# Kernel optimization log

Hardware: AMD Instinct MI355X
Metric: run time of the kernel (lower is better)

## Reference

```python
import jax, jax.numpy as jnp
import numpy as np

D_MODEL = 1024
NUM_HEADS = 16
HEAD_DIM = D_MODEL // NUM_HEADS
THETA = 10000.0
B, S = 4, 2048


def _rope(x, pos):
    # x: [B, H, S, d], pos: [B, S] int
    half = HEAD_DIM // 2
    inv_freq = THETA ** (-(jnp.arange(half, dtype=jnp.float32) * 2.0) / HEAD_DIM)  # [half]
    ang = pos.astype(jnp.float32)[:, None, :, None] * inv_freq  # [B, 1, S, half]
    cos, sin = jnp.cos(ang), jnp.sin(ang)
    x1, x2 = x[..., 0::2], x[..., 1::2]  # interleaved pairs
    r1 = x1 * cos - x2 * sin
    r2 = x1 * sin + x2 * cos
    return jnp.stack([r1, r2], axis=-1).reshape(x.shape)


def setup_inputs() -> dict:
    key = jax.random.key(0)
    ks = jax.random.split(key, 12)
    scale = 1.0 / np.sqrt(D_MODEL)
    inp = {
        "query": jax.random.normal(ks[0], (B, S, D_MODEL), dtype=jnp.float32),
        "key": jax.random.normal(ks[1], (B, S, D_MODEL), dtype=jnp.float32),
        "value": jax.random.normal(ks[2], (B, S, D_MODEL), dtype=jnp.float32),
        "token_positions": jnp.broadcast_to(jnp.arange(S, dtype=jnp.int32), (B, S)),
        "w_q": jax.random.normal(ks[3], (D_MODEL, D_MODEL), dtype=jnp.float32) * scale,
        "b_q": jnp.zeros((D_MODEL,), dtype=jnp.float32),
        "w_k": jax.random.normal(ks[4], (D_MODEL, D_MODEL), dtype=jnp.float32) * scale,
        "b_k": jnp.zeros((D_MODEL,), dtype=jnp.float32),
        "w_v": jax.random.normal(ks[5], (D_MODEL, D_MODEL), dtype=jnp.float32) * scale,
        "b_v": jnp.zeros((D_MODEL,), dtype=jnp.float32),
        "w_o": jax.random.normal(ks[6], (D_MODEL, D_MODEL), dtype=jnp.float32) * scale,
        "b_o": jnp.zeros((D_MODEL,), dtype=jnp.float32),
    }
    return inp


def reference(query, key, value, token_positions, w_q, b_q, w_k, b_k, w_v, b_v, w_o, b_o):
    b, s, _ = query.shape
    Q = query @ w_q + b_q
    K = key @ w_k + b_k
    V = value @ w_v + b_v
    # [B, S, H, d] -> [B, H, S, d]
    Q = Q.reshape(b, s, NUM_HEADS, HEAD_DIM).transpose(0, 2, 1, 3)
    K = K.reshape(b, s, NUM_HEADS, HEAD_DIM).transpose(0, 2, 1, 3)
    V = V.reshape(b, s, NUM_HEADS, HEAD_DIM).transpose(0, 2, 1, 3)
    Q = _rope(Q, token_positions)
    K = _rope(K, token_positions)
    scores = jnp.einsum("bhqd,bhkd->bhqk", Q, K) / jnp.sqrt(jnp.float32(HEAD_DIM))
    causal = jnp.tril(jnp.ones((s, s), dtype=bool))
    scores = jnp.where(causal, scores, -jnp.inf)
    attn = jax.nn.softmax(scores, axis=-1)
    out = jnp.einsum("bhqk,bhkd->bhqd", attn, V)
    out = out.transpose(0, 2, 1, 3).reshape(b, s, D_MODEL)
    return out @ w_o + b_o
```

## Files before the change

kernel.cpp:

```cpp
#include <hip/hip_runtime.h>

typedef __bf16 bf16;
typedef __attribute__((ext_vector_type(8))) __bf16 bf16x8;
typedef __attribute__((ext_vector_type(4))) __bf16 bf16x4;
typedef __attribute__((ext_vector_type(4))) float floatx4;

#define MFMA16(a, b, c) __builtin_amdgcn_mfma_f32_16x16x32_bf16((a), (b), (c), 0, 0, 0)

#define GLL(g, l)                                                   \
  __builtin_amdgcn_global_load_lds(                                 \
      (const __attribute__((address_space(1))) void*)(g),           \
      (__attribute__((address_space(3))) void*)(l), 16, 0, 0)

static constexpr int DM = 1024;
static constexpr int SEQ = 2048;
static constexpr int BATCH = 4;
static constexpr int NH = 16;
static constexpr int HD = 64;
static constexpr float LOG2E = 1.4426950408889634f;
static constexpr float LOG2_THETA = 13.287712379549449f;
static constexpr float QSC = 0.125f * LOG2E;

__global__ __launch_bounds__(256) void convert_x(
    const float* __restrict__ q, const float* __restrict__ k,
    const float* __restrict__ v, bf16* __restrict__ qo,
    bf16* __restrict__ ko, bf16* __restrict__ vo) {
  int z = blockIdx.z;
  const float* src = (z == 0) ? q : (z == 1) ? k : v;
  bf16* dst = (z == 0) ? qo : (z == 1) ? ko : vo;
  size_t i = ((size_t)blockIdx.x * blockDim.x + threadIdx.x) * 8;
  float4 a = *(const float4*)(src + i);
  float4 b = *(const float4*)(src + i + 4);
  bf16x8 o;
  o[0] = (bf16)a.x; o[1] = (bf16)a.y; o[2] = (bf16)a.z; o[3] = (bf16)a.w;
  o[4] = (bf16)b.x; o[5] = (bf16)b.y; o[6] = (bf16)b.z; o[7] = (bf16)b.w;
  *(bf16x8*)(dst + i) = o;
}

__global__ __launch_bounds__(256) void convert_w(
    const float* __restrict__ wq, const float* __restrict__ wk,
    const float* __restrict__ wv, const float* __restrict__ wo,
    bf16* __restrict__ oq, bf16* __restrict__ ok, bf16* __restrict__ ov,
    bf16* __restrict__ oo) {
  int z = blockIdx.z;
  const float* src = (z == 0) ? wq : (z == 1) ? wk : (z == 2) ? wv : wo;
  bf16* dst = (z == 0) ? oq : (z == 1) ? ok : (z == 2) ? ov : oo;
  __shared__ __align__(16) bf16 T[64][72];
  int k0 = blockIdx.y * 64, n0 = blockIdx.x * 64;
  int tid = threadIdx.x;
  int r = tid >> 4, c4 = (tid & 15) * 4;
#pragma unroll
  for (int i = 0; i < 4; i++) {
    int kk = r + i * 16;
    float4 v = *(const float4*)(src + (size_t)(k0 + kk) * DM + n0 + c4);
    T[c4 + 0][kk] = (bf16)v.x;
    T[c4 + 1][kk] = (bf16)v.y;
    T[c4 + 2][kk] = (bf16)v.z;
    T[c4 + 3][kk] = (bf16)v.w;
  }
  __syncthreads();
#pragma unroll
  for (int i = 0; i < 4; i++) {
    int nn = r + i * 16;
    bf16x4 o = *(const bf16x4*)&T[nn][c4];
    *(bf16x4*)(dst + (size_t)(n0 + nn) * DM + k0 + c4) = o;
  }
}

__global__ __launch_bounds__(256) void rope_table(const int* __restrict__ tp,
                                                  float* __restrict__ tab) {
  int idx = blockIdx.x * 256 + threadIdx.x;
  int m = idx >> 5, i = idx & 31;
  float pos = (float)tp[m];
  float invf = exp2f(-(float)(2 * i) * (LOG2_THETA / 64.0f));
  float s, c;
  sincosf(pos * invf, &s, &c);
  tab[(size_t)idx * 2] = c;
  tab[(size_t)idx * 2 + 1] = s;
}

__global__ __launch_bounds__(256) void gemm_qkv(
    const bf16* __restrict__ qb, const bf16* __restrict__ kb,
    const bf16* __restrict__ vb, const bf16* __restrict__ wqt,
    const bf16* __restrict__ wkt, const bf16* __restrict__ wvt,
    const float* __restrict__ biq, const float* __restrict__ bik,
    const float* __restrict__ biv, const float* __restrict__ tab,
    bf16* __restrict__ Qr, bf16* __restrict__ Kr, bf16* __restrict__ Vr) {
  int z = blockIdx.z;
  const bf16* X = (z == 0) ? qb : (z == 1) ? kb : vb;
  const bf16* Wt = (z == 0) ? wqt : (z == 1) ? wkt : wvt;
  const float* bias = (z == 0) ? biq : (z == 1) ? bik : biv;

  __shared__ __align__(16) bf16 As[128 * 64];
  __shared__ __align__(16) bf16 Bs[128 * 64];
  int lin = blockIdx.x;
  int m0 = (lin & 63) * 128, n0 = (lin >> 6) * 128;
  int tid = threadIdx.x;
  int lane = tid & 63, wv = tid >> 6;
  int quad = lane >> 4, low = lane & 15;
  int wm = (wv >> 1) * 64, wn = (wv & 1) * 64;
  int lr8 = lane >> 3;
  int swcol = ((lane & 7) ^ lr8) * 8;
  const bf16* AgL = X + (size_t)(m0 + wv * 8 + lr8) * DM + swcol;
  const bf16* BgL = Wt + (size_t)(n0 + wv * 8 + lr8) * DM + swcol;
  bf16* AsL = As + wv * 8 * 64;
  bf16* BsL = Bs + wv * 8 * 64;
  int r3 = low & 7;

  floatx4 acc[4][4];
#pragma unroll
  for (int i = 0; i < 4; i++)
#pragma unroll
    for (int j = 0; j < 4; j++) acc[i][j] = (floatx4)0.0f;

  for (int kt = 0; kt < DM; kt += 64) {
#pragma unroll
    for (int c = 0; c < 4; c++) {
      GLL(AgL + kt + (size_t)(c * 32) * DM, AsL + c * 2048);
      GLL(BgL + kt + (size_t)(c * 32) * DM, BsL + c * 2048);
    }
    __syncthreads();
#pragma unroll
    for (int kc = 0; kc < 2; kc++) {
      bf16x8 xf[4], wf[4];
#pragma unroll
      for (int t = 0; t < 4; t++)
        xf[t] = *(const bf16x8*)&As[(wm + t * 16 + low) * 64 +
                                    (((kc << 2) | quad) ^ r3) * 8];
#pragma unroll
      for (int t = 0; t < 4; t++)
        wf[t] = *(const bf16x8*)&Bs[(wn + t * 16 + low) * 64 +
                                    (((kc << 2) | quad) ^ r3) * 8];
#pragma unroll
      for (int i = 0; i < 4; i++)
#pragma unroll
        for (int j = 0; j < 4; j++)
          acc[i][j] = MFMA16(wf[i], xf[j], acc[i][j]);
    }
    __syncthreads();
  }

#pragma unroll
  for (int i = 0; i < 4; i++) {
    int nb = n0 + wn + i * 16 + quad * 4;
    float4 bv = *(const float4*)(bias + nb);
    int h = nb >> 6, dbase = nb & 63;
#pragma unroll
    for (int j = 0; j < 4; j++) {
      int m = m0 + wm + j * 16 + low;
      int bb = m >> 11, ss = m & 2047;
      float v0 = acc[i][j][0] + bv.x;
      float v1 = acc[i][j][1] + bv.y;
      float v2 = acc[i][j][2] + bv.z;
      float v3 = acc[i][j][3] + bv.w;
      size_t off = ((size_t)(bb * NH + h) * SEQ + ss) * HD + dbase;
      bf16x4 pk;
      if (z < 2) {
        float4 cs = *(const float4*)(tab + (size_t)m * 64 + dbase);
        float o0 = v0 * cs.x - v1 * cs.y;
        float o1 = v0 * cs.y + v1 * cs.x;
        float o2 = v2 * cs.z - v3 * cs.w;
        float o3 = v2 * cs.w + v3 * cs.z;
        if (z == 0) { o0 *= QSC; o1 *= QSC; o2 *= QSC; o3 *= QSC; }
        pk[0] = (bf16)o0; pk[1] = (bf16)o1;
        pk[2] = (bf16)o2; pk[3] = (bf16)o3;
        bf16* dst = (z == 0) ? Qr : Kr;
        *(bf16x4*)(dst + off) = pk;
      } else {
        pk[0] = (bf16)v0; pk[1] = (bf16)v1;
        pk[2] = (bf16)v2; pk[3] = (bf16)v3;
        *(bf16x4*)(Vr + off) = pk;
      }
    }
  }
}

__global__ __launch_bounds__(256) void transpose_v(const bf16* __restrict__ Vr,
                                                   bf16* __restrict__ Vt) {
  int bh = blockIdx.y;
  int s0 = blockIdx.x * 64;
  __shared__ __align__(16) bf16 T[64][72];
  int t = threadIdx.x;
  int r = t >> 2, c = (t & 3) * 16;
  const bf16* src = Vr + ((size_t)bh * SEQ + s0 + r) * HD + c;
  bf16x8 a = *(const bf16x8*)src;
  bf16x8 b = *(const bf16x8*)(src + 8);
  *(bf16x8*)&T[r][c] = a;
  *(bf16x8*)&T[r][c + 8] = b;
  __syncthreads();
  bf16* dst = Vt + ((size_t)bh * HD + r) * SEQ + s0 + c;
  bf16x8 o0, o1;
#pragma unroll
  for (int j = 0; j < 8; j++) {
    o0[j] = T[c + j][r];
    o1[j] = T[c + 8 + j][r];
  }
  *(bf16x8*)dst = o0;
  *(bf16x8*)(dst + 8) = o1;
}

__global__ __launch_bounds__(256, 3) void attn_fa(const bf16* __restrict__ Qr,
                                                  const bf16* __restrict__ Kr,
                                                  const bf16* __restrict__ Vt,
                                                  bf16* __restrict__ attn) {
  int lin = blockIdx.x;
  int bh = lin & 63, qi = 15 - (lin >> 6);
  int ntiles = 2 * qi + 2;
  int tid = threadIdx.x, lane = tid & 63, w = tid >> 6;
  int quad = lane >> 4, low = lane & 15;
  __shared__ __align__(16) bf16 Ks[2][64 * 72];
  __shared__ __align__(16) bf16 Vs[2][64 * 72];
  __shared__ __align__(16) bf16 Pl[4][16 * 72];
  const bf16* Qh = Qr + (size_t)bh * SEQ * HD;
  const bf16* Kh = Kr + (size_t)bh * SEQ * HD;
  const bf16* Vh = Vt + (size_t)bh * HD * SEQ;
  int bb = bh >> 4, h = bh & 15;
  int qrow0 = qi * 128 + w * 32;

  int sr = tid >> 2, scol = (tid & 3) * 16;
  const bf16* Kg = Kh + (size_t)sr * HD + scol;
  const bf16* Vg = Vh + (size_t)sr * SEQ + scol;
  int sl = sr * 72 + scol;

  bf16x8 ones;
#pragma unroll
  for (int j = 0; j < 8; j++) ones[j] = (bf16)1.0f;

  bf16x8 aq[2][2];
#pragma unroll
  for (int rt = 0; rt < 2; rt++)
#pragma unroll
    for (int kc = 0; kc < 2; kc++)
      aq[rt][kc] = *(const bf16x8*)(Qh + (size_t)(qrow0 + rt * 16 + low) * HD +
                                    kc * 32 + quad * 8);

  floatx4 accO[2][4];
  floatx4 lacc[2];
#pragma unroll
  for (int rt = 0; rt < 2; rt++) {
    lacc[rt] = (floatx4)0.0f;
#pragma unroll
    for (int nt = 0; nt < 4; nt++) accO[rt][nt] = (floatx4)0.0f;
  }

  {
    bf16x8 k0 = *(const bf16x8*)(Kg);
    bf16x8 k1 = *(const bf16x8*)(Kg + 8);
    bf16x8 v0 = *(const bf16x8*)(Vg);
    bf16x8 v1 = *(const bf16x8*)(Vg + 8);
    *(bf16x8*)&Ks[0][sl] = k0;
    *(bf16x8*)&Ks[0][sl + 8] = k1;
    *(bf16x8*)&Vs[0][sl] = v0;
    *(bf16x8*)&Vs[0][sl + 8] = v1;
  }
  __syncthreads();

  for (int kt = 0; kt < ntiles; kt++) {
    int cur = kt & 1;
    bf16x8 nk0, nk1, nv0, nv1;
    bool pre = (kt + 1 < ntiles);
    if (pre) {
      const bf16* kg = Kg + (size_t)(kt + 1) * (64 * HD);
      const bf16* vg = Vg + (size_t)(kt + 1) * 64;
      nk0 = *(const bf16x8*)(kg);
      nk1 = *(const bf16x8*)(kg + 8);
      nv0 = *(const bf16x8*)(vg);
      nv1 = *(const bf16x8*)(vg + 8);
    }

    floatx4 s2[2][4];
#pragma unroll
    for (int rt = 0; rt < 2; rt++)
#pragma unroll
      for (int nt = 0; nt < 4; nt++) s2[rt][nt] = (floatx4)0.0f;
#pragma unroll
    for (int nt = 0; nt < 4; nt++) {
      bf16x8 kb0 = *(const bf16x8*)&Ks[cur][(nt * 16 + low) * 72 + quad * 8];
      bf16x8 kb1 =
          *(const bf16x8*)&Ks[cur][(nt * 16 + low) * 72 + 32 + quad * 8];
#pragma unroll
      for (int rt = 0; rt < 2; rt++) {
        s2[rt][nt] = MFMA16(kb0, aq[rt][0], s2[rt][nt]);
        s2[rt][nt] = MFMA16(kb1, aq[rt][1], s2[rt][nt]);
      }
    }
    if (kt >= ntiles - 2) {
#pragma unroll
      for (int nt = 0; nt < 4; nt++)
#pragma unroll
        for (int r = 0; r < 4; r++) {
          int kg_ = kt * 64 + nt * 16 + quad * 4 + r;
#pragma unroll
          for (int rt = 0; rt < 2; rt++) {
            int qg = qrow0 + rt * 16 + low;
            if (kg_ > qg) s2[rt][nt][r] = -INFINITY;
          }
        }
    }
    bf16x4 pk[2][4];
#pragma unroll
    for (int rt = 0; rt < 2; rt++)
#pragma unroll
      for (int nt = 0; nt < 4; nt++)
#pragma unroll
        for (int r = 0; r < 4; r++)
          pk[rt][nt][r] = (bf16)exp2f(s2[rt][nt][r]);
    bf16x8 vb0[4], vb1[4];
#pragma unroll
    for (int nt = 0; nt < 4; nt++) {
      vb0[nt] = *(const bf16x8*)&Vs[cur][(nt * 16 + low) * 72 + quad * 8];
      vb1[nt] = *(const bf16x8*)&Vs[cur][(nt * 16 + low) * 72 + 32 + quad * 8];
    }
#pragma unroll
    for (int rt = 0; rt < 2; rt++) {
#pragma unroll
      for (int nt = 0; nt < 4; nt++)
        *(bf16x4*)&Pl[w][low * 72 + nt * 16 + quad * 4] = pk[rt][nt];
      asm volatile("s_waitcnt lgkmcnt(0)" ::: "memory");
      bf16x8 ap0 = *(const bf16x8*)&Pl[w][low * 72 + quad * 8];
      bf16x8 ap1 = *(const bf16x8*)&Pl[w][low * 72 + 32 + quad * 8];
#pragma unroll
      for (int nt = 0; nt < 4; nt++) {
        accO[rt][nt] = MFMA16(ap0, vb0[nt], accO[rt][nt]);
        accO[rt][nt] = MFMA16(ap1, vb1[nt], accO[rt][nt]);
      }
      lacc[rt] = MFMA16(ap0, ones, lacc[rt]);
      lacc[rt] = MFMA16(ap1, ones, lacc[rt]);
    }
    if (pre) {
      int nb = cur ^ 1;
      *(bf16x8*)&Ks[nb][sl] = nk0;
      *(bf16x8*)&Ks[nb][sl + 8] = nk1;
      *(bf16x8*)&Vs[nb][sl] = nv0;
      *(bf16x8*)&Vs[nb][sl + 8] = nv1;
    }
    __syncthreads();
  }

#pragma unroll
  for (int rt = 0; rt < 2; rt++)
#pragma unroll
    for (int r = 0; r < 4; r++) {
      float inv = 1.0f / lacc[rt][r];
      int q = qrow0 + rt * 16 + quad * 4 + r;
#pragma unroll
      for (int nt = 0; nt < 4; nt++) {
        float o = accO[rt][nt][r] * inv;
        attn[((size_t)(bb * SEQ + q)) * DM + h * HD + nt * 16 + low] = (bf16)o;
      }
    }
}

__global__ __launch_bounds__(256) void gemm_out(const bf16* __restrict__ X,
                                                const bf16* __restrict__ Wt,
                                                const float* __restrict__ bias,
                                                float* __restrict__ out) {
  __shared__ __align__(16) bf16 As[128 * 64];
  __shared__ __align__(16) bf16 Bs[128 * 64];
  int lin = blockIdx.x;
  int m0 = (lin & 63) * 128, n0 = (lin >> 6) * 128;
  int tid = threadIdx.x;
  int lane = tid & 63, wv = tid >> 6;
  int quad = lane >> 4, low = lane & 15;
  int wm = (wv >> 1) * 64, wn = (wv & 1) * 64;
  int lr8 = lane >> 3;
  int swcol = ((lane & 7) ^ lr8) * 8;
  const bf16* AgL = X + (size_t)(m0 + wv * 8 + lr8) * DM + swcol;
  const bf16* BgL = Wt + (size_t)(n0 + wv * 8 + lr8) * DM + swcol;
  bf16* AsL = As + wv * 8 * 64;
  bf16* BsL = Bs + wv * 8 * 64;
  int r3 = low & 7;

  floatx4 acc[4][4];
#pragma unroll
  for (int i = 0; i < 4; i++)
#pragma unroll
    for (int j = 0; j < 4; j++) acc[i][j] = (floatx4)0.0f;

  for (int kt = 0; kt < DM; kt += 64) {
#pragma unroll
    for (int c = 0; c < 4; c++) {
      GLL(AgL + kt + (size_t)(c * 32) * DM, AsL + c * 2048);
      GLL(BgL + kt + (size_t)(c * 32) * DM, BsL + c * 2048);
    }
    __syncthreads();
#pragma unroll
    for (int kc = 0; kc < 2; kc++) {
      bf16x8 xf[4], wf[4];
#pragma unroll
      for (int t = 0; t < 4; t++)
        xf[t] = *(const bf16x8*)&As[(wm + t * 16 + low) * 64 +
                                    (((kc << 2) | quad) ^ r3) * 8];
#pragma unroll
      for (int t = 0; t < 4; t++)
        wf[t] = *(const bf16x8*)&Bs[(wn + t * 16 + low) * 64 +
                                    (((kc << 2) | quad) ^ r3) * 8];
#pragma unroll
      for (int i = 0; i < 4; i++)
#pragma unroll
        for (int j = 0; j < 4; j++)
          acc[i][j] = MFMA16(wf[i], xf[j], acc[i][j]);
    }
    __syncthreads();
  }

#pragma unroll
  for (int i = 0; i < 4; i++) {
    int nb = n0 + wn + i * 16 + quad * 4;
    float4 bv = *(const float4*)(bias + nb);
#pragma unroll
    for (int j = 0; j < 4; j++) {
      int m = m0 + wm + j * 16 + low;
      float4 o;
      o.x = acc[i][j][0] + bv.x;
      o.y = acc[i][j][1] + bv.y;
      o.z = acc[i][j][2] + bv.z;
      o.w = acc[i][j][3] + bv.w;
      *(float4*)(out + (size_t)m * DM + nb) = o;
    }
  }
}

extern "C" void kernel_launch(void* const* d_in, const int* in_sizes, int n_in,
                              void* d_out, int out_size, void* d_ws,
                              size_t ws_size, hipStream_t stream) {
  const float* query = (const float*)d_in[0];
  const float* key_ = (const float*)d_in[1];
  const float* value = (const float*)d_in[2];
  const int* tp = (const int*)d_in[3];
  const float* w_q = (const float*)d_in[4];
  const float* b_q = (const float*)d_in[5];
  const float* w_k = (const float*)d_in[6];
  const float* b_k = (const float*)d_in[7];
  const float* w_v = (const float*)d_in[8];
  const float* b_v = (const float*)d_in[9];
  const float* w_o = (const float*)d_in[10];
  const float* b_o = (const float*)d_in[11];

  char* w = (char*)d_ws;
  const size_t MB = 1u << 20;
  bf16* qb = (bf16*)(w + 0);
  bf16* kb = (bf16*)(w + 16 * MB);
  bf16* vb = (bf16*)(w + 32 * MB);
  bf16* wqt = (bf16*)(w + 48 * MB);
  bf16* wkt = (bf16*)(w + 50 * MB);
  bf16* wvt = (bf16*)(w + 52 * MB);
  bf16* wot = (bf16*)(w + 54 * MB);
  bf16* Qr = (bf16*)(w + 56 * MB);
  bf16* Kr = (bf16*)(w + 72 * MB);
  bf16* Vr = (bf16*)(w + 88 * MB);
  float* tab = (float*)(w + 104 * MB);
  bf16* Vt = (bf16*)(w + 32 * MB);
  bf16* attnb = (bf16*)(w + 0);

  convert_x<<<dim3(4096, 1, 3), 256, 0, stream>>>(query, key_, value, qb, kb,
                                                  vb);
  convert_w<<<dim3(16, 16, 4), 256, 0, stream>>>(w_q, w_k, w_v, w_o, wqt, wkt,
                                                 wvt, wot);
  rope_table<<<1024, 256, 0, stream>>>(tp, tab);
  gemm_qkv<<<dim3(512, 1, 3), 256, 0, stream>>>(qb, kb, vb, wqt, wkt, wvt,
                                                b_q, b_k, b_v, tab, Qr, Kr,
                                                Vr);
  transpose_v<<<dim3(32, 64), 256, 0, stream>>>(Vr, Vt);
  attn_fa<<<dim3(1024), 256, 0, stream>>>(Qr, Kr, Vt, attnb);
  gemm_out<<<dim3(512), 256, 0, stream>>>(attnb, wot, b_o, (float*)d_out);
}
```

Baseline: 330.8 us.

## Triple-buffer GEMM tiles with async LDS prefetch and larger 256x128 blocks

Replaces the single-buffered GEMM loop in the QKV and output projections with a shared gemm_core. It keeps three LDS stages and issues global_load_lds prefetches two k-tiles ahead, split across the two half-k steps. Explicit vmcnt/lgkmcnt waits, s_barrier and setprio bracket the MFMA blocks so that loads overlap compute. Block size grows to 512 threads with a 256x128 tile, which halves the grid and increases reuse of the weight tile. The cost is about 144KB of LDS per block, so only one block fits per CU, and the tile count now roughly matches the CU count, which risks load imbalance and low occupancy.

```diff
diff --git a/kernel.cpp b/kernel.cpp
--- a/kernel.cpp
+++ b/kernel.cpp
@@ -17,6 +17,7 @@
 static constexpr int BATCH = 4;
 static constexpr int NH = 16;
 static constexpr int HD = 64;
+static constexpr int NT = DM / 64;
 static constexpr float LOG2E = 1.4426950408889634f;
 static constexpr float LOG2_THETA = 13.287712379549449f;
 static constexpr float QSC = 0.125f * LOG2E;
@@ -79,7 +80,114 @@
   tab[(size_t)idx * 2 + 1] = s;
 }
 
-__global__ __launch_bounds__(256) void gemm_qkv(
+__device__ __forceinline__ void gemm_core(const bf16* __restrict__ X,
+                                          const bf16* __restrict__ Wt,
+                                          bf16* As, bf16* Bs, int m0, int n0,
+                                          int tid, floatx4 acc[4][4]) {
+  int lane = tid & 63, wvq = tid >> 6;
+  int quad = lane >> 4, low = lane & 15;
+  int wm = (wvq >> 1) * 64, wn = (wvq & 1) * 64;
+  int lr8 = lane >> 3;
+  int swcol = ((lane & 7) ^ lr8) * 8;
+  const bf16* AgL = X + (size_t)(m0 + wvq * 8 + lr8) * DM + swcol;
+  const bf16* BgL = Wt + (size_t)(n0 + wvq * 8 + lr8) * DM + swcol;
+  bf16* AsW = As + wvq * 512;
+  bf16* BsW = Bs + wvq * 512;
+  int r3 = low & 7;
+
+#define GQ_A(kt2, b, r)                                            \
+  GLL(AgL + (size_t)(kt2) * 64 + (size_t)(r) * 64 * DM,            \
+      AsW + (b) * 16384 + (r) * 4096)
+#define GQ_B(kt2, b, r)                                            \
+  GLL(BgL + (size_t)(kt2) * 64 + (size_t)(r) * 64 * DM,            \
+      BsW + (b) * 8192 + (r) * 4096)
+
+#pragma unroll
+  for (int i = 0; i < 4; i++)
+#pragma unroll
+    for (int j = 0; j < 4; j++) acc[i][j] = (floatx4)0.0f;
+
+#pragma unroll
+  for (int r = 0; r < 4; r++) GQ_A(0, 0, r);
+#pragma unroll
+  for (int r = 0; r < 2; r++) GQ_B(0, 0, r);
+#pragma unroll
+  for (int r = 0; r < 4; r++) GQ_A(1, 1, r);
+#pragma unroll
+  for (int r = 0; r < 2; r++) GQ_B(1, 1, r);
+  asm volatile("s_waitcnt vmcnt(6)" ::: "memory");
+  __builtin_amdgcn_s_barrier();
+
+  int rb = 0;
+  for (int t = 0; t < NT; ++t) {
+    int sb = rb + 2;
+    if (sb > 2) sb -= 3;
+    const bf16* Ab = As + rb * 16384;
+    const bf16* Bb = Bs + rb * 8192;
+    bool st = (t < NT - 2);
+    bf16x8 wf[4], xf[4];
+#pragma unroll
+    for (int i = 0; i < 4; i++)
+      wf[i] = *(const bf16x8*)&Bb[(wn + i * 16 + low) * 64 + (quad ^ r3) * 8];
+#pragma unroll
+    for (int j = 0; j < 4; j++)
+      xf[j] = *(const bf16x8*)&Ab[(wm + j * 16 + low) * 64 + (quad ^ r3) * 8];
+    if (st) {
+      GQ_A(t + 2, sb, 0);
+      GQ_A(t + 2, sb, 1);
+      GQ_B(t + 2, sb, 0);
+    }
+    __builtin_amdgcn_sched_barrier(0);
+    __builtin_amdgcn_s_barrier();
+    asm volatile("s_waitcnt lgkmcnt(0)" ::: "memory");
+    __builtin_amdgcn_sched_barrier(0);
+    __builtin_amdgcn_s_setprio(1);
+#pragma unroll
+    for (int i = 0; i < 4; i++)
+#pragma unroll
+      for (int j = 0; j < 4; j++)
+        acc[i][j] = MFMA16(wf[i], xf[j], acc[i][j]);
+    __builtin_amdgcn_s_setprio(0);
+    __builtin_amdgcn_sched_barrier(0);
+    __builtin_amdgcn_s_barrier();
+#pragma unroll
+    for (int i = 0; i < 4; i++)
+      wf[i] =
+          *(const bf16x8*)&Bb[(wn + i * 16 + low) * 64 + ((4 | quad) ^ r3) * 8];
+#pragma unroll
+    for (int j = 0; j < 4; j++)
+      xf[j] =
+          *(const bf16x8*)&Ab[(wm + j * 16 + low) * 64 + ((4 | quad) ^ r3) * 8];
+    if (st) {
+      GQ_A(t + 2, sb, 2);
+      GQ_A(t + 2, sb, 3);
+      GQ_B(t + 2, sb, 1);
+    }
+    __builtin_amdgcn_sched_barrier(0);
+    __builtin_amdgcn_s_barrier();
+    asm volatile("s_waitcnt lgkmcnt(0)" ::: "memory");
+    __builtin_amdgcn_sched_barrier(0);
+    __builtin_amdgcn_s_setprio(1);
+#pragma unroll
+    for (int i = 0; i < 4; i++)
+#pragma unroll
+      for (int j = 0; j < 4; j++)
+        acc[i][j] = MFMA16(wf[i], xf[j], acc[i][j]);
+    __builtin_amdgcn_s_setprio(0);
+    if (st)
+      asm volatile("s_waitcnt vmcnt(6)" ::: "memory");
+    else
+      asm volatile("s_waitcnt vmcnt(0)" ::: "memory");
+    __builtin_amdgcn_sched_barrier(0);
+    __builtin_amdgcn_s_barrier();
+    rb = rb + 1;
+    if (rb > 2) rb -= 3;
+  }
+#undef GQ_A
+#undef GQ_B
+}
+
+__global__ __launch_bounds__(512) void gemm_qkv(
     const bf16* __restrict__ qb, const bf16* __restrict__ kb,
     const bf16* __restrict__ vb, const bf16* __restrict__ wqt,
     const bf16* __restrict__ wkt, const bf16* __restrict__ wvt,
@@ -91,54 +199,18 @@
   const bf16* Wt = (z == 0) ? wqt : (z == 1) ? wkt : wvt;
   const float* bias = (z == 0) ? biq : (z == 1) ? bik : biv;
 
-  __shared__ __align__(16) bf16 As[128 * 64];
-  __shared__ __align__(16) bf16 Bs[128 * 64];
+  __shared__ __align__(16) bf16 As[3 * 256 * 64];
+  __shared__ __align__(16) bf16 Bs[3 * 128 * 64];
   int lin = blockIdx.x;
-  int m0 = (lin & 63) * 128, n0 = (lin >> 6) * 128;
+  int m0 = (lin & 31) * 256, n0 = (lin >> 5) * 128;
   int tid = threadIdx.x;
-  int lane = tid & 63, wv = tid >> 6;
+
+  floatx4 acc[4][4];
+  gemm_core(X, Wt, As, Bs, m0, n0, tid, acc);
+
+  int lane = tid & 63, wvq = tid >> 6;
   int quad = lane >> 4, low = lane & 15;
-  int wm = (wv >> 1) * 64, wn = (wv & 1) * 64;
-  int lr8 = lane >> 3;
-  int swcol = ((lane & 7) ^ lr8) * 8;
-  const bf16* AgL = X + (size_t)(m0 + wv * 8 + lr8) * DM + swcol;
-  const bf16* BgL = Wt + (size_t)(n0 + wv * 8 + lr8) * DM + swcol;
-  bf16* AsL = As + wv * 8 * 64;
-  bf16* BsL = Bs + wv * 8 * 64;
-  int r3 = low & 7;
-
-  floatx4 acc[4][4];
-#pragma unroll
-  for (int i = 0; i < 4; i++)
-#pragma unroll
-    for (int j = 0; j < 4; j++) acc[i][j] = (floatx4)0.0f;
-
-  for (int kt = 0; kt < DM; kt += 64) {
-#pragma unroll
-    for (int c = 0; c < 4; c++) {
-      GLL(AgL + kt + (size_t)(c * 32) * DM, AsL + c * 2048);
-      GLL(BgL + kt + (size_t)(c * 32) * DM, BsL + c * 2048);
-    }
-    __syncthreads();
-#pragma unroll
-    for (int kc = 0; kc < 2; kc++) {
-      bf16x8 xf[4], wf[4];
-#pragma unroll
-      for (int t = 0; t < 4; t++)
-        xf[t] = *(const bf16x8*)&As[(wm + t * 16 + low) * 64 +
-                                    (((kc << 2) | quad) ^ r3) * 8];
-#pragma unroll
-      for (int t = 0; t < 4; t++)
-        wf[t] = *(const bf16x8*)&Bs[(wn + t * 16 + low) * 64 +
-                                    (((kc << 2) | quad) ^ r3) * 8];
-#pragma unroll
-      for (int i = 0; i < 4; i++)
-#pragma unroll
-        for (int j = 0; j < 4; j++)
-          acc[i][j] = MFMA16(wf[i], xf[j], acc[i][j]);
-    }
-    __syncthreads();
-  }
+  int wm = (wvq >> 1) * 64, wn = (wvq & 1) * 64;
 
 #pragma unroll
   for (int i = 0; i < 4; i++) {
@@ -351,58 +423,22 @@
     }
 }
 
-__global__ __launch_bounds__(256) void gemm_out(const bf16* __restrict__ X,
+__global__ __launch_bounds__(512) void gemm_out(const bf16* __restrict__ X,
                                                 const bf16* __restrict__ Wt,
                                                 const float* __restrict__ bias,
                                                 float* __restrict__ out) {
-  __shared__ __align__(16) bf16 As[128 * 64];
-  __shared__ __align__(16) bf16 Bs[128 * 64];
+  __shared__ __align__(16) bf16 As[3 * 256 * 64];
+  __shared__ __align__(16) bf16 Bs[3 * 128 * 64];
   int lin = blockIdx.x;
-  int m0 = (lin & 63) * 128, n0 = (lin >> 6) * 128;
+  int m0 = (lin & 31) * 256, n0 = (lin >> 5) * 128;
   int tid = threadIdx.x;
-  int lane = tid & 63, wv = tid >> 6;
+
+  floatx4 acc[4][4];
+  gemm_core(X, Wt, As, Bs, m0, n0, tid, acc);
+
+  int lane = tid & 63, wvq = tid >> 6;
   int quad = lane >> 4, low = lane & 15;
-  int wm = (wv >> 1) * 64, wn = (wv & 1) * 64;
-  int lr8 = lane >> 3;
-  int swcol = ((lane & 7) ^ lr8) * 8;
-  const bf16* AgL = X + (size_t)(m0 + wv * 8 + lr8) * DM + swcol;
-  const bf16* BgL = Wt + (size_t)(n0 + wv * 8 + lr8) * DM + swcol;
-  bf16* AsL = As + wv * 8 * 64;
-  bf16* BsL = Bs + wv * 8 * 64;
-  int r3 = low & 7;
-
-  floatx4 acc[4][4];
-#pragma unroll
-  for (int i = 0; i < 4; i++)
-#pragma unroll
-    for (int j = 0; j < 4; j++) acc[i][j] = (floatx4)0.0f;
-
-  for (int kt = 0; kt < DM; kt += 64) {
-#pragma unroll
-    for (int c = 0; c < 4; c++) {
-      GLL(AgL + kt + (size_t)(c * 32) * DM, AsL + c * 2048);
-      GLL(BgL + kt + (size_t)(c * 32) * DM, BsL + c * 2048);
-    }
-    __syncthreads();
-#pragma unroll
-    for (int kc = 0; kc < 2; kc++) {
-      bf16x8 xf[4], wf[4];
-#pragma unroll
-      for (int t = 0; t < 4; t++)
-        xf[t] = *(const bf16x8*)&As[(wm + t * 16 + low) * 64 +
-                                    (((kc << 2) | quad) ^ r3) * 8];
-#pragma unroll
-      for (int t = 0; t < 4; t++)
-        wf[t] = *(const bf16x8*)&Bs[(wn + t * 16 + low) * 64 +
-                                    (((kc << 2) | quad) ^ r3) * 8];
-#pragma unroll
-      for (int i = 0; i < 4; i++)
-#pragma unroll
-        for (int j = 0; j < 4; j++)
-          acc[i][j] = MFMA16(wf[i], xf[j], acc[i][j]);
-    }
-    __syncthreads();
-  }
+  int wm = (wvq >> 1) * 64, wn = (wvq & 1) * 64;
 
 #pragma unroll
   for (int i = 0; i < 4; i++) {
@@ -458,10 +494,10 @@
   convert_w<<<dim3(16, 16, 4), 256, 0, stream>>>(w_q, w_k, w_v, w_o, wqt, wkt,
                                                  wvt, wot);
   rope_table<<<1024, 256, 0, stream>>>(tp, tab);
-  gemm_qkv<<<dim3(512, 1, 3), 256, 0, stream>>>(qb, kb, vb, wqt, wkt, wvt,
+  gemm_qkv<<<dim3(256, 1, 3), 512, 0, stream>>>(qb, kb, vb, wqt, wkt, wvt,
                                                 b_q, b_k, b_v, tab, Qr, Kr,
                                                 Vr);
   transpose_v<<<dim3(32, 64), 256, 0, stream>>>(Vr, Vt);
   attn_fa<<<dim3(1024), 256, 0, stream>>>(Qr, Kr, Vt, attnb);
-  gemm_out<<<dim3(512), 256, 0, stream>>>(attnb, wot, b_o, (float*)d_out);
-}
+  gemm_out<<<dim3(256), 512, 0, stream>>>(attnb, wot, b_o, (float*)d_out);
+}
```

After: 330.1 us. Within noise of the previous version (-0.2%).

## Merge prep kernels into one launch and fuse V transpose into QKV epilogue

Applied to the files above, without the earlier changes.

Merges the three preprocessing kernels (input conversion, weight transpose-convert, rope table) into a single launch that dispatches work by block index. The V projection epilogue now stages its tile through shared memory with an XOR swizzle and writes V directly in transposed [bh, d, seq] layout, so the separate transpose kernel and its extra global round trip go away. The cost is more shared-memory traffic, an extra barrier in the V branch of the GEMM epilogue, and a branchy prep kernel.

```diff
diff --git a/kernel.cpp b/kernel.cpp
--- a/kernel.cpp
+++ b/kernel.cpp
@@ -21,62 +21,62 @@
 static constexpr float LOG2_THETA = 13.287712379549449f;
 static constexpr float QSC = 0.125f * LOG2E;
 
-__global__ __launch_bounds__(256) void convert_x(
+__global__ __launch_bounds__(256) void prep(
     const float* __restrict__ q, const float* __restrict__ k,
     const float* __restrict__ v, bf16* __restrict__ qo,
-    bf16* __restrict__ ko, bf16* __restrict__ vo) {
-  int z = blockIdx.z;
-  const float* src = (z == 0) ? q : (z == 1) ? k : v;
-  bf16* dst = (z == 0) ? qo : (z == 1) ? ko : vo;
-  size_t i = ((size_t)blockIdx.x * blockDim.x + threadIdx.x) * 8;
-  float4 a = *(const float4*)(src + i);
-  float4 b = *(const float4*)(src + i + 4);
-  bf16x8 o;
-  o[0] = (bf16)a.x; o[1] = (bf16)a.y; o[2] = (bf16)a.z; o[3] = (bf16)a.w;
-  o[4] = (bf16)b.x; o[5] = (bf16)b.y; o[6] = (bf16)b.z; o[7] = (bf16)b.w;
-  *(bf16x8*)(dst + i) = o;
-}
-
-__global__ __launch_bounds__(256) void convert_w(
+    bf16* __restrict__ ko, bf16* __restrict__ vo,
     const float* __restrict__ wq, const float* __restrict__ wk,
     const float* __restrict__ wv, const float* __restrict__ wo,
     bf16* __restrict__ oq, bf16* __restrict__ ok, bf16* __restrict__ ov,
-    bf16* __restrict__ oo) {
-  int z = blockIdx.z;
-  const float* src = (z == 0) ? wq : (z == 1) ? wk : (z == 2) ? wv : wo;
-  bf16* dst = (z == 0) ? oq : (z == 1) ? ok : (z == 2) ? ov : oo;
+    bf16* __restrict__ oo, const int* __restrict__ tp,
+    float* __restrict__ tab) {
   __shared__ __align__(16) bf16 T[64][72];
-  int k0 = blockIdx.y * 64, n0 = blockIdx.x * 64;
+  int bid = blockIdx.x;
   int tid = threadIdx.x;
-  int r = tid >> 4, c4 = (tid & 15) * 4;
-#pragma unroll
-  for (int i = 0; i < 4; i++) {
-    int kk = r + i * 16;
-    float4 v = *(const float4*)(src + (size_t)(k0 + kk) * DM + n0 + c4);
-    T[c4 + 0][kk] = (bf16)v.x;
-    T[c4 + 1][kk] = (bf16)v.y;
-    T[c4 + 2][kk] = (bf16)v.z;
-    T[c4 + 3][kk] = (bf16)v.w;
-  }
-  __syncthreads();
-#pragma unroll
-  for (int i = 0; i < 4; i++) {
-    int nn = r + i * 16;
-    bf16x4 o = *(const bf16x4*)&T[nn][c4];
-    *(bf16x4*)(dst + (size_t)(n0 + nn) * DM + k0 + c4) = o;
-  }
-}
-
-__global__ __launch_bounds__(256) void rope_table(const int* __restrict__ tp,
-                                                  float* __restrict__ tab) {
-  int idx = blockIdx.x * 256 + threadIdx.x;
-  int m = idx >> 5, i = idx & 31;
-  float pos = (float)tp[m];
-  float invf = exp2f(-(float)(2 * i) * (LOG2_THETA / 64.0f));
-  float s, c;
-  sincosf(pos * invf, &s, &c);
-  tab[(size_t)idx * 2] = c;
-  tab[(size_t)idx * 2 + 1] = s;
+  if (bid < 12288) {
+    int z = bid >> 12, x = bid & 4095;
+    const float* src = (z == 0) ? q : (z == 1) ? k : v;
+    bf16* dst = (z == 0) ? qo : (z == 1) ? ko : vo;
+    size_t i = ((size_t)x * 256 + tid) * 8;
+    float4 a = *(const float4*)(src + i);
+    float4 b = *(const float4*)(src + i + 4);
+    bf16x8 o;
+    o[0] = (bf16)a.x; o[1] = (bf16)a.y; o[2] = (bf16)a.z; o[3] = (bf16)a.w;
+    o[4] = (bf16)b.x; o[5] = (bf16)b.y; o[6] = (bf16)b.z; o[7] = (bf16)b.w;
+    *(bf16x8*)(dst + i) = o;
+  } else if (bid < 13312) {
+    int b2 = bid - 12288;
+    int z = b2 >> 8, yy = (b2 >> 4) & 15, xx = b2 & 15;
+    const float* src = (z == 0) ? wq : (z == 1) ? wk : (z == 2) ? wv : wo;
+    bf16* dst = (z == 0) ? oq : (z == 1) ? ok : (z == 2) ? ov : oo;
+    int k0 = yy * 64, n0 = xx * 64;
+    int r = tid >> 4, c4 = (tid & 15) * 4;
+#pragma unroll
+    for (int i = 0; i < 4; i++) {
+      int kk = r + i * 16;
+      float4 vv = *(const float4*)(src + (size_t)(k0 + kk) * DM + n0 + c4);
+      T[c4 + 0][kk] = (bf16)vv.x;
+      T[c4 + 1][kk] = (bf16)vv.y;
+      T[c4 + 2][kk] = (bf16)vv.z;
+      T[c4 + 3][kk] = (bf16)vv.w;
+    }
+    __syncthreads();
+#pragma unroll
+    for (int i = 0; i < 4; i++) {
+      int nn = r + i * 16;
+      bf16x4 o = *(const bf16x4*)&T[nn][c4];
+      *(bf16x4*)(dst + (size_t)(n0 + nn) * DM + k0 + c4) = o;
+    }
+  } else {
+    int idx = (bid - 13312) * 256 + tid;
+    int m = idx >> 5, i = idx & 31;
+    float pos = (float)tp[m];
+    float invf = exp2f(-(float)(2 * i) * (LOG2_THETA / 64.0f));
+    float s, c;
+    sincosf(pos * invf, &s, &c);
+    tab[(size_t)idx * 2] = c;
+    tab[(size_t)idx * 2 + 1] = s;
+  }
 }
 
 __global__ __launch_bounds__(256) void gemm_qkv(
@@ -85,26 +85,27 @@
     const bf16* __restrict__ wkt, const bf16* __restrict__ wvt,
     const float* __restrict__ biq, const float* __restrict__ bik,
     const float* __restrict__ biv, const float* __restrict__ tab,
-    bf16* __restrict__ Qr, bf16* __restrict__ Kr, bf16* __restrict__ Vr) {
+    bf16* __restrict__ Qr, bf16* __restrict__ Kr, bf16* __restrict__ Vt) {
   int z = blockIdx.z;
   const bf16* X = (z == 0) ? qb : (z == 1) ? kb : vb;
   const bf16* Wt = (z == 0) ? wqt : (z == 1) ? wkt : wvt;
   const float* bias = (z == 0) ? biq : (z == 1) ? bik : biv;
 
-  __shared__ __align__(16) bf16 As[128 * 64];
-  __shared__ __align__(16) bf16 Bs[128 * 64];
+  __shared__ __align__(16) bf16 SM[2 * 128 * 64];
+  bf16* As = SM;
+  bf16* Bs = SM + 128 * 64;
   int lin = blockIdx.x;
   int m0 = (lin & 63) * 128, n0 = (lin >> 6) * 128;
   int tid = threadIdx.x;
-  int lane = tid & 63, wv = tid >> 6;
+  int lane = tid & 63, wvx = tid >> 6;
   int quad = lane >> 4, low = lane & 15;
-  int wm = (wv >> 1) * 64, wn = (wv & 1) * 64;
+  int wm = (wvx >> 1) * 64, wn = (wvx & 1) * 64;
   int lr8 = lane >> 3;
   int swcol = ((lane & 7) ^ lr8) * 8;
-  const bf16* AgL = X + (size_t)(m0 + wv * 8 + lr8) * DM + swcol;
-  const bf16* BgL = Wt + (size_t)(n0 + wv * 8 + lr8) * DM + swcol;
-  bf16* AsL = As + wv * 8 * 64;
-  bf16* BsL = Bs + wv * 8 * 64;
+  const bf16* AgL = X + (size_t)(m0 + wvx * 8 + lr8) * DM + swcol;
+  const bf16* BgL = Wt + (size_t)(n0 + wvx * 8 + lr8) * DM + swcol;
+  bf16* AsL = As + wvx * 8 * 64;
+  bf16* BsL = Bs + wvx * 8 * 64;
   int r3 = low & 7;
 
   floatx4 acc[4][4];
@@ -140,63 +141,67 @@
     __syncthreads();
   }
 
-#pragma unroll
-  for (int i = 0; i < 4; i++) {
-    int nb = n0 + wn + i * 16 + quad * 4;
-    float4 bv = *(const float4*)(bias + nb);
-    int h = nb >> 6, dbase = nb & 63;
-#pragma unroll
-    for (int j = 0; j < 4; j++) {
-      int m = m0 + wm + j * 16 + low;
-      int bb = m >> 11, ss = m & 2047;
-      float v0 = acc[i][j][0] + bv.x;
-      float v1 = acc[i][j][1] + bv.y;
-      float v2 = acc[i][j][2] + bv.z;
-      float v3 = acc[i][j][3] + bv.w;
-      size_t off = ((size_t)(bb * NH + h) * SEQ + ss) * HD + dbase;
-      bf16x4 pk;
-      if (z < 2) {
+  if (z < 2) {
+#pragma unroll
+    for (int i = 0; i < 4; i++) {
+      int nb = n0 + wn + i * 16 + quad * 4;
+      float4 bv = *(const float4*)(bias + nb);
+      int h = nb >> 6, dbase = nb & 63;
+#pragma unroll
+      for (int j = 0; j < 4; j++) {
+        int m = m0 + wm + j * 16 + low;
+        int bb = m >> 11, ss = m & 2047;
+        float v0 = acc[i][j][0] + bv.x;
+        float v1 = acc[i][j][1] + bv.y;
+        float v2 = acc[i][j][2] + bv.z;
+        float v3 = acc[i][j][3] + bv.w;
+        size_t off = ((size_t)(bb * NH + h) * SEQ + ss) * HD + dbase;
         float4 cs = *(const float4*)(tab + (size_t)m * 64 + dbase);
         float o0 = v0 * cs.x - v1 * cs.y;
         float o1 = v0 * cs.y + v1 * cs.x;
         float o2 = v2 * cs.z - v3 * cs.w;
         float o3 = v2 * cs.w + v3 * cs.z;
         if (z == 0) { o0 *= QSC; o1 *= QSC; o2 *= QSC; o3 *= QSC; }
+        bf16x4 pk;
         pk[0] = (bf16)o0; pk[1] = (bf16)o1;
         pk[2] = (bf16)o2; pk[3] = (bf16)o3;
         bf16* dst = (z == 0) ? Qr : Kr;
         *(bf16x4*)(dst + off) = pk;
-      } else {
-        pk[0] = (bf16)v0; pk[1] = (bf16)v1;
-        pk[2] = (bf16)v2; pk[3] = (bf16)v3;
-        *(bf16x4*)(Vr + off) = pk;
       }
     }
-  }
-}
-
-__global__ __launch_bounds__(256) void transpose_v(const bf16* __restrict__ Vr,
-                                                   bf16* __restrict__ Vt) {
-  int bh = blockIdx.y;
-  int s0 = blockIdx.x * 64;
-  __shared__ __align__(16) bf16 T[64][72];
-  int t = threadIdx.x;
-  int r = t >> 2, c = (t & 3) * 16;
-  const bf16* src = Vr + ((size_t)bh * SEQ + s0 + r) * HD + c;
-  bf16x8 a = *(const bf16x8*)src;
-  bf16x8 b = *(const bf16x8*)(src + 8);
-  *(bf16x8*)&T[r][c] = a;
-  *(bf16x8*)&T[r][c + 8] = b;
-  __syncthreads();
-  bf16* dst = Vt + ((size_t)bh * HD + r) * SEQ + s0 + c;
-  bf16x8 o0, o1;
-#pragma unroll
-  for (int j = 0; j < 8; j++) {
-    o0[j] = T[c + j][r];
-    o1[j] = T[c + 8 + j][r];
-  }
-  *(bf16x8*)dst = o0;
-  *(bf16x8*)(dst + 8) = o1;
+  } else {
+#pragma unroll
+    for (int i = 0; i < 4; i++) {
+      int nbl = wn + i * 16 + quad * 4;
+      float4 bv = *(const float4*)(bias + n0 + nbl);
+#pragma unroll
+      for (int j = 0; j < 4; j++) {
+        int m = wm + j * 16 + low;
+        float vv0 = acc[i][j][0] + bv.x;
+        float vv1 = acc[i][j][1] + bv.y;
+        float vv2 = acc[i][j][2] + bv.z;
+        float vv3 = acc[i][j][3] + bv.w;
+        int swb = (m >> 3);
+        int e = m & 7;
+        SM[(nbl + 0) * 128 + (swb ^ ((nbl + 0) & 15)) * 8 + e] = (bf16)vv0;
+        SM[(nbl + 1) * 128 + (swb ^ ((nbl + 1) & 15)) * 8 + e] = (bf16)vv1;
+        SM[(nbl + 2) * 128 + (swb ^ ((nbl + 2) & 15)) * 8 + e] = (bf16)vv2;
+        SM[(nbl + 3) * 128 + (swb ^ ((nbl + 3) & 15)) * 8 + e] = (bf16)vv3;
+      }
+    }
+    __syncthreads();
+    int n_loc = tid >> 1, half = tid & 1;
+    int n_g = n0 + n_loc;
+    int h = n_g >> 6, d = n_g & 63;
+    int bb = m0 >> 11, s0 = (m0 & 2047) + half * 64;
+    bf16* dst = Vt + ((size_t)(bb * NH + h) * HD + d) * SEQ + s0;
+#pragma unroll
+    for (int c = 0; c < 8; c++) {
+      int chunk = (half * 8 + c) ^ (n_loc & 15);
+      bf16x8 o = *(const bf16x8*)&SM[n_loc * 128 + chunk * 8];
+      *(bf16x8*)(dst + c * 8) = o;
+    }
+  }
 }
 
 __global__ __launch_bounds__(256, 3) void attn_fa(const bf16* __restrict__ Qr,
@@ -360,15 +365,15 @@
   int lin = blockIdx.x;
   int m0 = (lin & 63) * 128, n0 = (lin >> 6) * 128;
   int tid = threadIdx.x;
-  int lane = tid & 63, wv = tid >> 6;
+  int lane = tid & 63, wvx = tid >> 6;
   int quad = lane >> 4, low = lane & 15;
-  int wm = (wv >> 1) * 64, wn = (wv & 1) * 64;
+  int wm = (wvx >> 1) * 64, wn = (wvx & 1) * 64;
   int lr8 = lane >> 3;
   int swcol = ((lane & 7) ^ lr8) * 8;
-  const bf16* AgL = X + (size_t)(m0 + wv * 8 + lr8) * DM + swcol;
-  const bf16* BgL = Wt + (size_t)(n0 + wv * 8 + lr8) * DM + swcol;
-  bf16* AsL = As + wv * 8 * 64;
-  bf16* BsL = Bs + wv * 8 * 64;
+  const bf16* AgL = X + (size_t)(m0 + wvx * 8 + lr8) * DM + swcol;
+  const bf16* BgL = Wt + (size_t)(n0 + wvx * 8 + lr8) * DM + swcol;
+  bf16* AsL = As + wvx * 8 * 64;
+  bf16* BsL = Bs + wvx * 8 * 64;
   int r3 = low & 7;
 
   floatx4 acc[4][4];
@@ -448,20 +453,16 @@
   bf16* wot = (bf16*)(w + 54 * MB);
   bf16* Qr = (bf16*)(w + 56 * MB);
   bf16* Kr = (bf16*)(w + 72 * MB);
-  bf16* Vr = (bf16*)(w + 88 * MB);
+  bf16* Vt = (bf16*)(w + 88 * MB);
   float* tab = (float*)(w + 104 * MB);
-  bf16* Vt = (bf16*)(w + 32 * MB);
   bf16* attnb = (bf16*)(w + 0);
 
-  convert_x<<<dim3(4096, 1, 3), 256, 0, stream>>>(query, key_, value, qb, kb,
-                                                  vb);
-  convert_w<<<dim3(16, 16, 4), 256, 0, stream>>>(w_q, w_k, w_v, w_o, wqt, wkt,
-                                                 wvt, wot);
-  rope_table<<<1024, 256, 0, stream>>>(tp, tab);
+  prep<<<dim3(14336), 256, 0, stream>>>(query, key_, value, qb, kb, vb, w_q,
+                                        w_k, w_v, w_o, wqt, wkt, wvt, wot, tp,
+                                        tab);
   gemm_qkv<<<dim3(512, 1, 3), 256, 0, stream>>>(qb, kb, vb, wqt, wkt, wvt,
                                                 b_q, b_k, b_v, tab, Qr, Kr,
-                                                Vr);
-  transpose_v<<<dim3(32, 64), 256, 0, stream>>>(Vr, Vt);
+                                                Vt);
   attn_fa<<<dim3(1024), 256, 0, stream>>>(Qr, Kr, Vt, attnb);
   gemm_out<<<dim3(512), 256, 0, stream>>>(attnb, wot, b_o, (float*)d_out);
 }
```

After: 362.2 us. 1.09x slower.

## Merge prep kernels, stage P in spare K buffer, raise MFMA priority

Applied to the files above, without the earlier changes.

Folds the input conversion, weight transpose-conversion and RoPE table kernels into a single launch that branches on block index, removing two kernel launches and their gaps. In the attention kernel, the per-wave P staging buffer is dropped. P is now written into the not-yet-refilled half of the double-buffered K tile, where each wave's rows line up with the rows it later overwrites with its own prefetch. This cuts LDS use per block. The MFMA sections are also wrapped in s_setprio to favour matrix issue across waves. The aliasing depends on the prefetch row mapping matching the wave's P rows, which makes the buffer reuse fragile to future layout changes.

```diff
diff --git a/kernel.cpp b/kernel.cpp
--- a/kernel.cpp
+++ b/kernel.cpp
@@ -21,62 +21,62 @@
 static constexpr float LOG2_THETA = 13.287712379549449f;
 static constexpr float QSC = 0.125f * LOG2E;
 
-__global__ __launch_bounds__(256) void convert_x(
+__global__ __launch_bounds__(256) void prep(
     const float* __restrict__ q, const float* __restrict__ k,
     const float* __restrict__ v, bf16* __restrict__ qo,
-    bf16* __restrict__ ko, bf16* __restrict__ vo) {
-  int z = blockIdx.z;
-  const float* src = (z == 0) ? q : (z == 1) ? k : v;
-  bf16* dst = (z == 0) ? qo : (z == 1) ? ko : vo;
-  size_t i = ((size_t)blockIdx.x * blockDim.x + threadIdx.x) * 8;
-  float4 a = *(const float4*)(src + i);
-  float4 b = *(const float4*)(src + i + 4);
-  bf16x8 o;
-  o[0] = (bf16)a.x; o[1] = (bf16)a.y; o[2] = (bf16)a.z; o[3] = (bf16)a.w;
-  o[4] = (bf16)b.x; o[5] = (bf16)b.y; o[6] = (bf16)b.z; o[7] = (bf16)b.w;
-  *(bf16x8*)(dst + i) = o;
-}
-
-__global__ __launch_bounds__(256) void convert_w(
+    bf16* __restrict__ ko, bf16* __restrict__ vo,
     const float* __restrict__ wq, const float* __restrict__ wk,
     const float* __restrict__ wv, const float* __restrict__ wo,
     bf16* __restrict__ oq, bf16* __restrict__ ok, bf16* __restrict__ ov,
-    bf16* __restrict__ oo) {
-  int z = blockIdx.z;
-  const float* src = (z == 0) ? wq : (z == 1) ? wk : (z == 2) ? wv : wo;
-  bf16* dst = (z == 0) ? oq : (z == 1) ? ok : (z == 2) ? ov : oo;
+    bf16* __restrict__ oo, const int* __restrict__ tp,
+    float* __restrict__ tab) {
   __shared__ __align__(16) bf16 T[64][72];
-  int k0 = blockIdx.y * 64, n0 = blockIdx.x * 64;
+  int bid = blockIdx.x;
   int tid = threadIdx.x;
-  int r = tid >> 4, c4 = (tid & 15) * 4;
-#pragma unroll
-  for (int i = 0; i < 4; i++) {
-    int kk = r + i * 16;
-    float4 v = *(const float4*)(src + (size_t)(k0 + kk) * DM + n0 + c4);
-    T[c4 + 0][kk] = (bf16)v.x;
-    T[c4 + 1][kk] = (bf16)v.y;
-    T[c4 + 2][kk] = (bf16)v.z;
-    T[c4 + 3][kk] = (bf16)v.w;
-  }
-  __syncthreads();
-#pragma unroll
-  for (int i = 0; i < 4; i++) {
-    int nn = r + i * 16;
-    bf16x4 o = *(const bf16x4*)&T[nn][c4];
-    *(bf16x4*)(dst + (size_t)(n0 + nn) * DM + k0 + c4) = o;
-  }
-}
-
-__global__ __launch_bounds__(256) void rope_table(const int* __restrict__ tp,
-                                                  float* __restrict__ tab) {
-  int idx = blockIdx.x * 256 + threadIdx.x;
-  int m = idx >> 5, i = idx & 31;
-  float pos = (float)tp[m];
-  float invf = exp2f(-(float)(2 * i) * (LOG2_THETA / 64.0f));
-  float s, c;
-  sincosf(pos * invf, &s, &c);
-  tab[(size_t)idx * 2] = c;
-  tab[(size_t)idx * 2 + 1] = s;
+  if (bid < 12288) {
+    int z = bid >> 12, x = bid & 4095;
+    const float* src = (z == 0) ? q : (z == 1) ? k : v;
+    bf16* dst = (z == 0) ? qo : (z == 1) ? ko : vo;
+    size_t i = ((size_t)x * 256 + tid) * 8;
+    float4 a = *(const float4*)(src + i);
+    float4 b = *(const float4*)(src + i + 4);
+    bf16x8 o;
+    o[0] = (bf16)a.x; o[1] = (bf16)a.y; o[2] = (bf16)a.z; o[3] = (bf16)a.w;
+    o[4] = (bf16)b.x; o[5] = (bf16)b.y; o[6] = (bf16)b.z; o[7] = (bf16)b.w;
+    *(bf16x8*)(dst + i) = o;
+  } else if (bid < 13312) {
+    int b2 = bid - 12288;
+    int z = b2 >> 8, yy = (b2 >> 4) & 15, xx = b2 & 15;
+    const float* src = (z == 0) ? wq : (z == 1) ? wk : (z == 2) ? wv : wo;
+    bf16* dst = (z == 0) ? oq : (z == 1) ? ok : (z == 2) ? ov : oo;
+    int k0 = yy * 64, n0 = xx * 64;
+    int r = tid >> 4, c4 = (tid & 15) * 4;
+#pragma unroll
+    for (int i = 0; i < 4; i++) {
+      int kk = r + i * 16;
+      float4 vv = *(const float4*)(src + (size_t)(k0 + kk) * DM + n0 + c4);
+      T[c4 + 0][kk] = (bf16)vv.x;
+      T[c4 + 1][kk] = (bf16)vv.y;
+      T[c4 + 2][kk] = (bf16)vv.z;
+      T[c4 + 3][kk] = (bf16)vv.w;
+    }
+    __syncthreads();
+#pragma unroll
+    for (int i = 0; i < 4; i++) {
+      int nn = r + i * 16;
+      bf16x4 o = *(const bf16x4*)&T[nn][c4];
+      *(bf16x4*)(dst + (size_t)(n0 + nn) * DM + k0 + c4) = o;
+    }
+  } else {
+    int idx = (bid - 13312) * 256 + tid;
+    int m = idx >> 5, i = idx & 31;
+    float pos = (float)tp[m];
+    float invf = exp2f(-(float)(2 * i) * (LOG2_THETA / 64.0f));
+    float s, c;
+    sincosf(pos * invf, &s, &c);
+    tab[(size_t)idx * 2] = c;
+    tab[(size_t)idx * 2 + 1] = s;
+  }
 }
 
 __global__ __launch_bounds__(256) void gemm_qkv(
@@ -210,7 +210,6 @@
   int quad = lane >> 4, low = lane & 15;
   __shared__ __align__(16) bf16 Ks[2][64 * 72];
   __shared__ __align__(16) bf16 Vs[2][64 * 72];
-  __shared__ __align__(16) bf16 Pl[4][16 * 72];
   const bf16* Qh = Qr + (size_t)bh * SEQ * HD;
   const bf16* Kh = Kr + (size_t)bh * SEQ * HD;
   const bf16* Vh = Vt + (size_t)bh * HD * SEQ;
@@ -257,6 +256,7 @@
 
   for (int kt = 0; kt < ntiles; kt++) {
     int cur = kt & 1;
+    bf16* Pw = &Ks[cur ^ 1][(w * 16) * 72];
     bf16x8 nk0, nk1, nv0, nv1;
     bool pre = (kt + 1 < ntiles);
     if (pre) {
@@ -273,6 +273,7 @@
     for (int rt = 0; rt < 2; rt++)
 #pragma unroll
       for (int nt = 0; nt < 4; nt++) s2[rt][nt] = (floatx4)0.0f;
+    __builtin_amdgcn_s_setprio(1);
 #pragma unroll
     for (int nt = 0; nt < 4; nt++) {
       bf16x8 kb0 = *(const bf16x8*)&Ks[cur][(nt * 16 + low) * 72 + quad * 8];
@@ -284,6 +285,7 @@
         s2[rt][nt] = MFMA16(kb1, aq[rt][1], s2[rt][nt]);
       }
     }
+    __builtin_amdgcn_s_setprio(0);
     if (kt >= ntiles - 2) {
 #pragma unroll
       for (int nt = 0; nt < 4; nt++)
@@ -315,10 +317,11 @@
     for (int rt = 0; rt < 2; rt++) {
 #pragma unroll
       for (int nt = 0; nt < 4; nt++)
-        *(bf16x4*)&Pl[w][low * 72 + nt * 16 + quad * 4] = pk[rt][nt];
+        *(bf16x4*)&Pw[low * 72 + nt * 16 + quad * 4] = pk[rt][nt];
       asm volatile("s_waitcnt lgkmcnt(0)" ::: "memory");
-      bf16x8 ap0 = *(const bf16x8*)&Pl[w][low * 72 + quad * 8];
-      bf16x8 ap1 = *(const bf16x8*)&Pl[w][low * 72 + 32 + quad * 8];
+      bf16x8 ap0 = *(const bf16x8*)&Pw[low * 72 + quad * 8];
+      bf16x8 ap1 = *(const bf16x8*)&Pw[low * 72 + 32 + quad * 8];
+      __builtin_amdgcn_s_setprio(1);
 #pragma unroll
       for (int nt = 0; nt < 4; nt++) {
         accO[rt][nt] = MFMA16(ap0, vb0[nt], accO[rt][nt]);
@@ -326,6 +329,7 @@
       }
       lacc[rt] = MFMA16(ap0, ones, lacc[rt]);
       lacc[rt] = MFMA16(ap1, ones, lacc[rt]);
+      __builtin_amdgcn_s_setprio(0);
     }
     if (pre) {
       int nb = cur ^ 1;
@@ -453,11 +457,9 @@
   bf16* Vt = (bf16*)(w + 32 * MB);
   bf16* attnb = (bf16*)(w + 0);
 
-  convert_x<<<dim3(4096, 1, 3), 256, 0, stream>>>(query, key_, value, qb, kb,
-                                                  vb);
-  convert_w<<<dim3(16, 16, 4), 256, 0, stream>>>(w_q, w_k, w_v, w_o, wqt, wkt,
-                                                 wvt, wot);
-  rope_table<<<1024, 256, 0, stream>>>(tp, tab);
+  prep<<<dim3(14336), 256, 0, stream>>>(query, key_, value, qb, kb, vb, w_q,
+                                        w_k, w_v, w_o, wqt, wkt, wvt, wot, tp,
+                                        tab);
   gemm_qkv<<<dim3(512, 1, 3), 256, 0, stream>>>(qb, kb, vb, wqt, wkt, wvt,
                                                 b_q, b_k, b_v, tab, Qr, Kr,
                                                 Vr);
```

Result: faster. 322.5 us (-2.5%).
